# Kernel optimization log

Measured on AMD Instinct MI355X. Metric: run time of the kernel, lower is better.

Reference implementation:

```python
import jax, jax.numpy as jnp
import numpy as np

ENC, STR_H, CELL_H, ATTN = 512, 256, 512, 512
B, L = 64, 1024


def setup_inputs() -> dict:
    key = jax.random.key(0)
    ks = jax.random.split(key, 12)
    s = lambda fan_in: 1.0 / np.sqrt(fan_in)
    return {
        "encoded_features_map": jax.random.normal(ks[0], (B, L, ENC), jnp.float32),
        "structural_hidden_state": jax.random.normal(ks[1], (1, B, STR_H), jnp.float32),
        "cell_content_hidden_state": jax.random.normal(ks[2], (1, B, CELL_H), jnp.float32),
        "W_enc": jax.random.uniform(ks[3], (ENC, ATTN), jnp.float32, -s(ENC), s(ENC)),
        "b_enc": jax.random.uniform(ks[4], (ATTN,), jnp.float32, -s(ENC), s(ENC)),
        "W_str": jax.random.uniform(ks[5], (STR_H, ATTN), jnp.float32, -s(STR_H), s(STR_H)),
        "b_str": jax.random.uniform(ks[6], (ATTN,), jnp.float32, -s(STR_H), s(STR_H)),
        "W_cell": jax.random.uniform(ks[7], (CELL_H, ATTN), jnp.float32, -s(CELL_H), s(CELL_H)),
        "b_cell": jax.random.uniform(ks[8], (ATTN,), jnp.float32, -s(CELL_H), s(CELL_H)),
        "W_comb": jax.random.uniform(ks[9], (ATTN, 1), jnp.float32, -s(ATTN), s(ATTN)),
        "b_comb": jax.random.uniform(ks[10], (1,), jnp.float32, -s(ATTN), s(ATTN)),
    }


def reference(encoded_features_map, structural_hidden_state, cell_content_hidden_state,
              W_enc, b_enc, W_str, b_str, W_cell, b_cell, W_comb, b_comb):
    # [B, L, A] projection of encoder features
    a_enc = jnp.einsum("ble,ea->bla", encoded_features_map, W_enc) + b_enc
    # [B, A] projections of the two hidden states (squeeze layer dim)
    a_str = structural_hidden_state[0] @ W_str + b_str
    a_cell = cell_content_hidden_state[0] @ W_cell + b_cell
    # broadcast add + ReLU + scalar score: [B, L]
    h = jax.nn.relu(a_enc + a_str[:, None, :] + a_cell[:, None, :])
    scores = jnp.einsum("bla,ao->bl", h, W_comb) + b_comb[0]
    weights = jax.nn.softmax(scores, axis=1)  # over sequence dim
    # weighted sum over L -> [B, ENC]
    context = jnp.einsum("bl,ble->be", weights, encoded_features_map)
    return context
```

## Files before the change

kernel.cpp:

```cpp
#include <hip/hip_runtime.h>
#include <stdint.h>

#define ENC_D 512
#define ATTN_D 512
#define STR_D 256
#define CELL_D 512
#define BATCH 64
#define SEQ 1024
#define NROWS (BATCH * SEQ)

typedef __bf16 bf16x8 __attribute__((ext_vector_type(8)));
typedef float f32x4 __attribute__((ext_vector_type(4)));

__device__ __forceinline__ unsigned short f2bf(float f) {
    unsigned int u = __float_as_uint(f);
    u += 0x7fffu + ((u >> 16) & 1u);
    return (unsigned short)(u >> 16);
}

__device__ __forceinline__ void lds_cp16(void* l, const void* g) {
    __builtin_amdgcn_global_load_lds(
        (const __attribute__((address_space(1))) unsigned int*)g,
        (__attribute__((address_space(3))) unsigned int*)l, 16, 0, 0);
}

#define BAR_VM4() asm volatile("s_waitcnt vmcnt(4)\n\ts_barrier" ::: "memory")

__global__ __launch_bounds__(256) void k_prep(const float* __restrict__ W,
                                              unsigned short* __restrict__ WF,
                                              const float* __restrict__ str,
                                              const float* __restrict__ cell,
                                              const float* __restrict__ Wstr,
                                              const float* __restrict__ Wcell,
                                              float* __restrict__ bpart) {
    __shared__ char smraw[64 * 68 * 2];
    const int bx = blockIdx.x, t = threadIdx.x;

    if (bx < 64) {
        unsigned short* T = (unsigned short*)smraw;
        const int ei = bx >> 3, ni = bx & 7;
        const int e0 = ei * 64, n0 = ni * 64;
#pragma unroll
        for (int i = 0; i < 4; ++i) {
            const int idx = t + i * 256;
            const int r = idx >> 4, c4 = idx & 15;
            const float4 v = *(const float4*)(W + (size_t)(e0 + r) * ATTN_D + n0 + c4 * 4);
            T[(c4 * 4 + 0) * 68 + r] = f2bf(v.x);
            T[(c4 * 4 + 1) * 68 + r] = f2bf(v.y);
            T[(c4 * 4 + 2) * 68 + r] = f2bf(v.z);
            T[(c4 * 4 + 3) * 68 + r] = f2bf(v.w);
        }
        __syncthreads();
#pragma unroll
        for (int i = 0; i < 2; ++i) {
            const int q = t + i * 256;
            const int n = q >> 3, ge = q & 7;
            union { unsigned short s[8]; uint4 u; } o;
#pragma unroll
            for (int j = 0; j < 8; ++j) o.s[j] = T[n * 68 + ge * 8 + j];
            const int ng = n0 + n;
            const int g = ei * 8 + ge;
            const int nt = ng >> 4, c = ng & 15;
            const int ks = g >> 2, quad = g & 3;
            const int gi = ks * 2048 + nt * 64 + quad * 16 + c;
            *(uint4*)(WF + (size_t)gi * 8) = o.u;
        }
    } else {
        float* sj = (float*)smraw;
        float* red = (float*)smraw + 64;
        const int q = bx - 64;
        const int b = q / 12, jq = q - b * 12;
        const float* hvec;
        const float* Wbase;
        if (jq < 4) { hvec = str + b * STR_D + jq * 64;         Wbase = Wstr + (size_t)(jq * 64) * ATTN_D; }
        else        { hvec = cell + b * CELL_D + (jq - 4) * 64; Wbase = Wcell + (size_t)((jq - 4) * 64) * ATTN_D; }
        if (t < 64) sj[t] = hvec[t];
        __syncthreads();
        const int h = t >> 7, a4 = t & 127;
        f32x4 acc = {0.f, 0.f, 0.f, 0.f};
#pragma unroll 8
        for (int i = h * 32; i < h * 32 + 32; ++i) {
            const float s = sj[i];
            const float4 wv = *(const float4*)(Wbase + (size_t)i * ATTN_D + a4 * 4);
            acc[0] += s * wv.x; acc[1] += s * wv.y; acc[2] += s * wv.z; acc[3] += s * wv.w;
        }
        if (h == 1) *(f32x4*)(red + a4 * 4) = acc;
        __syncthreads();
        if (h == 0) {
            const f32x4 o = *(const f32x4*)(red + a4 * 4);
            acc[0] += o[0]; acc[1] += o[1]; acc[2] += o[2]; acc[3] += o[3];
            *(f32x4*)(bpart + (size_t)(jq * BATCH + b) * ATTN_D + a4 * 4) = acc;
        }
    }
}

__global__ __launch_bounds__(512, 2) void k_scores(const float* __restrict__ E,
                                                   const unsigned short* __restrict__ WF,
                                                   const float* __restrict__ bpart,
                                                   const float* __restrict__ b_enc,
                                                   const float* __restrict__ b_str,
                                                   const float* __restrict__ b_cell,
                                                   const float* __restrict__ Wcomb,
                                                   float* __restrict__ ctxp,
                                                   float* __restrict__ stats) {
    __shared__ unsigned short buf[3][16384];
    __shared__ float sbias[512];
    __shared__ float sWc[512];
    __shared__ float sxp[4][128];
    __shared__ float sx[128];
    __shared__ float ex[128];
    __shared__ float red[3][512];
    __shared__ float rtmp[4];

    const int tid = threadIdx.x;
    const int r0 = blockIdx.x * 128;
    const int b = blockIdx.x >> 3;
    const int w = tid >> 6, lane = tid & 63;
    const int wm = w >> 2, wn = w & 3;
    const int quad = lane >> 4, c = lane & 15;

#pragma unroll
    for (int p = 0; p < 2; ++p)
#pragma unroll
        for (int i = 0; i < 4; ++i)
            lds_cp16((char*)&buf[p][0] + i * 8192 + tid * 16,
                     (const char*)WF + (size_t)p * 32768 + i * 8192 + tid * 16);

    if (tid < 128) {
        const int a = tid * 4;
        const float4 be = *(const float4*)(b_enc + a);
        const float4 bs = *(const float4*)(b_str + a);
        const float4 bc = *(const float4*)(b_cell + a);
        f32x4 s;
        s[0] = be.x + bs.x + bc.x; s[1] = be.y + bs.y + bc.y;
        s[2] = be.z + bs.z + bc.z; s[3] = be.w + bs.w + bc.w;
#pragma unroll
        for (int jq = 0; jq < 12; ++jq) {
            const float4 p = *(const float4*)(bpart + (size_t)(jq * BATCH + b) * ATTN_D + a);
            s[0] += p.x; s[1] += p.y; s[2] += p.z; s[3] += p.w;
        }
        *(f32x4*)(sbias + a) = s;
        const float4 wcv = *(const float4*)(Wcomb + a);
        f32x4 wc4; wc4[0] = wcv.x; wc4[1] = wcv.y; wc4[2] = wcv.z; wc4[3] = wcv.w;
        *(f32x4*)(sWc + a) = wc4;
    }

    f32x4 acc[4][8];
#pragma unroll
    for (int mt = 0; mt < 4; ++mt)
#pragma unroll
        for (int nt = 0; nt < 8; ++nt) {
            const f32x4 z = {0.f, 0.f, 0.f, 0.f};
            acc[mt][nt] = z;
        }

    __syncthreads();

    const float* Ebase = E + (size_t)(r0 + wm * 64 + c) * ENC_D + quad * 8;

    int cbuf = 0, sbuf = 2;
    for (int ch = 0; ch < 16; ++ch) {
        float4 v0[4], v1[4];
#pragma unroll
        for (int mt = 0; mt < 4; ++mt) {
            const float* Ep = Ebase + (size_t)(mt * 16) * ENC_D + ch * 32;
            v0[mt] = *(const float4*)(Ep);
            v1[mt] = *(const float4*)(Ep + 4);
        }

        if (ch < 14) {
            const char* gsrc = (const char*)WF + (size_t)(ch + 2) * 32768;
            char* ldst = (char*)&buf[sbuf][0];
#pragma unroll
            for (int i = 0; i < 4; ++i)
                lds_cp16(ldst + i * 8192 + tid * 16, gsrc + i * 8192 + tid * 16);
        }

        bf16x8 av[4];
#pragma unroll
        for (int mt = 0; mt < 4; ++mt) {
            union { unsigned short s[8]; bf16x8 v; } u;
            u.s[0] = f2bf(v0[mt].x); u.s[1] = f2bf(v0[mt].y);
            u.s[2] = f2bf(v0[mt].z); u.s[3] = f2bf(v0[mt].w);
            u.s[4] = f2bf(v1[mt].x); u.s[5] = f2bf(v1[mt].y);
            u.s[6] = f2bf(v1[mt].z); u.s[7] = f2bf(v1[mt].w);
            av[mt] = u.v;
        }

        const unsigned short* wb = &buf[cbuf][0];
        bf16x8 bfr[8];
#pragma unroll
        for (int nt = 0; nt < 8; ++nt)
            bfr[nt] = *(const bf16x8*)(wb + ((wn * 8 + nt) * 64 + lane) * 8);
#pragma unroll
        for (int nt = 0; nt < 8; ++nt)
#pragma unroll
            for (int mt = 0; mt < 4; ++mt)
                acc[mt][nt] = __builtin_amdgcn_mfma_f32_16x16x32_bf16(av[mt], bfr[nt], acc[mt][nt], 0, 0, 0);

        cbuf = (cbuf == 2) ? 0 : cbuf + 1;
        sbuf = (sbuf == 2) ? 0 : sbuf + 1;
        if (ch < 15) BAR_VM4();
    }

    float sp[4][4];
#pragma unroll
    for (int mt = 0; mt < 4; ++mt)
#pragma unroll
        for (int reg = 0; reg < 4; ++reg) sp[mt][reg] = 0.f;
#pragma unroll
    for (int nt = 0; nt < 8; ++nt) {
        const int col = wn * 128 + nt * 16 + c;
        const float bi = sbias[col], wc = sWc[col];
#pragma unroll
        for (int mt = 0; mt < 4; ++mt)
#pragma unroll
            for (int reg = 0; reg < 4; ++reg) {
                const float v = acc[mt][nt][reg] + bi;
                sp[mt][reg] += (v > 0.f ? v : 0.f) * wc;
            }
    }
#pragma unroll
    for (int mt = 0; mt < 4; ++mt)
#pragma unroll
        for (int reg = 0; reg < 4; ++reg) {
            float v = sp[mt][reg];
            v += __shfl_xor(v, 1);
            v += __shfl_xor(v, 2);
            v += __shfl_xor(v, 4);
            v += __shfl_xor(v, 8);
            sp[mt][reg] = v;
        }
    if (c == 0) {
#pragma unroll
        for (int mt = 0; mt < 4; ++mt)
#pragma unroll
            for (int reg = 0; reg < 4; ++reg)
                sxp[wn][wm * 64 + mt * 16 + quad * 4 + reg] = sp[mt][reg];
    }
    __syncthreads();

    if (tid < 128)
        sx[tid] = sxp[0][tid] + sxp[1][tid] + sxp[2][tid] + sxp[3][tid];

    if (tid < 128) {
        float mm = sx[tid];
#pragma unroll
        for (int o = 32; o > 0; o >>= 1) mm = fmaxf(mm, __shfl_xor(mm, o));
        if (lane == 0) rtmp[w] = mm;
    }
    __syncthreads();
    const float m_p = fmaxf(rtmp[0], rtmp[1]);
    if (tid < 128) {
        const float e = __expf(sx[tid] - m_p);
        ex[tid] = e;
        float ss = e;
#pragma unroll
        for (int o = 32; o > 0; o >>= 1) ss += __shfl_xor(ss, o);
        if (lane == 0) rtmp[2 + w] = ss;
    }
    __syncthreads();
    if (tid == 0) {
        stats[blockIdx.x * 2 + 0] = m_p;
        stats[blockIdx.x * 2 + 1] = rtmp[2] + rtmp[3];
    }

    {
        const int g = tid >> 7, col4 = tid & 127;
        const float* Ep = E + (size_t)(r0 + g * 32) * ENC_D + col4 * 4;
        f32x4 a4 = {0.f, 0.f, 0.f, 0.f};
#pragma unroll 8
        for (int l = 0; l < 32; ++l) {
            const float4 e4 = *(const float4*)(Ep + (size_t)l * ENC_D);
            const float wgt = ex[g * 32 + l];
            a4[0] += wgt * e4.x; a4[1] += wgt * e4.y;
            a4[2] += wgt * e4.z; a4[3] += wgt * e4.w;
        }
        if (g > 0) *(f32x4*)(&red[g - 1][col4 * 4]) = a4;
        __syncthreads();
        if (g == 0) {
            const f32x4 r1 = *(const f32x4*)(&red[0][col4 * 4]);
            const f32x4 r2 = *(const f32x4*)(&red[1][col4 * 4]);
            const f32x4 r3 = *(const f32x4*)(&red[2][col4 * 4]);
            a4[0] += r1[0] + r2[0] + r3[0];
            a4[1] += r1[1] + r2[1] + r3[1];
            a4[2] += r1[2] + r2[2] + r3[2];
            a4[3] += r1[3] + r2[3] + r3[3];
            *(f32x4*)(ctxp + (size_t)blockIdx.x * 512 + col4 * 4) = a4;
        }
    }
}

__global__ __launch_bounds__(128) void k_final(const float* __restrict__ ctxp,
                                               const float* __restrict__ stats,
                                               float* __restrict__ out) {
    const int b = blockIdx.x, t = threadIdx.x;
    float mp[8], zp[8];
    float m = -1e30f;
#pragma unroll
    for (int p = 0; p < 8; ++p) {
        mp[p] = stats[(b * 8 + p) * 2];
        zp[p] = stats[(b * 8 + p) * 2 + 1];
        m = fmaxf(m, mp[p]);
    }
    float D = 0.f;
    float a[8];
#pragma unroll
    for (int p = 0; p < 8; ++p) { a[p] = __expf(mp[p] - m); D += zp[p] * a[p]; }
    const float invD = 1.f / D;

    f32x4 o = {0.f, 0.f, 0.f, 0.f};
#pragma unroll
    for (int p = 0; p < 8; ++p) {
        const float4 cp = *(const float4*)(ctxp + (size_t)(b * 8 + p) * 512 + t * 4);
        o[0] += cp.x * a[p]; o[1] += cp.y * a[p];
        o[2] += cp.z * a[p]; o[3] += cp.w * a[p];
    }
    o[0] *= invD; o[1] *= invD; o[2] *= invD; o[3] *= invD;
    *(f32x4*)(out + (size_t)b * ENC_D + t * 4) = o;
}

extern "C" void kernel_launch(void* const* d_in, const int* in_sizes, int n_in,
                              void* d_out, int out_size, void* d_ws, size_t ws_size,
                              hipStream_t stream) {
    const float* E      = (const float*)d_in[0];
    const float* str    = (const float*)d_in[1];
    const float* cell   = (const float*)d_in[2];
    const float* Wenc   = (const float*)d_in[3];
    const float* b_enc  = (const float*)d_in[4];
    const float* Wstr   = (const float*)d_in[5];
    const float* b_str  = (const float*)d_in[6];
    const float* Wcell  = (const float*)d_in[7];
    const float* b_cell = (const float*)d_in[8];
    const float* Wcomb  = (const float*)d_in[9];
    float* out = (float*)d_out;

    char* ws = (char*)d_ws;
    unsigned short* WF = (unsigned short*)ws;
    float* bpart = (float*)(ws + (512 << 10));
    float* ctxp  = (float*)(ws + (512 << 10) + (1536 << 10));
    float* stats = (float*)(ws + (512 << 10) + (2560 << 10));

    k_prep<<<832, 256, 0, stream>>>(Wenc, WF, str, cell, Wstr, Wcell, bpart);
    k_scores<<<NROWS / 128, 512, 0, stream>>>(E, WF, bpart, b_enc, b_str, b_cell, Wcomb, ctxp, stats);
    k_final<<<BATCH, 128, 0, stream>>>(ctxp, stats, out);
}
```

Before: 286.3 us.

## Double-buffer encoder activations in registers and use native bf16 conversion

Restructures the k_scores main loop so each chunk's fp32 encoder rows are loaded one chunk ahead into alternating register sets, and the loop is unrolled by two via a macro. The intent is to hide global load latency behind the MFMA work of the current chunk. The manual round-to-nearest-even bf16 packing is replaced with native `__bf16` casts to cut ALU work. The explicit `s_waitcnt vmcnt(4)` before the barrier is dropped and only a bare `s_barrier` remains, leaving LDS-DMA completion ordering to compiler-inserted waits. This risks a race on the weight staging buffers and raises register pressure from the extra prefetch registers.

After: 284.3 us. Within noise of the previous version (-0.7%).

```diff
diff --git a/kernel.cpp b/kernel.cpp
--- a/kernel.cpp
+++ b/kernel.cpp
@@ -18,13 +18,20 @@
     return (unsigned short)(u >> 16);
 }
 
+__device__ __forceinline__ bf16x8 cvt8(const float4 a, const float4 b) {
+    bf16x8 r;
+    r[0] = (__bf16)a.x; r[1] = (__bf16)a.y; r[2] = (__bf16)a.z; r[3] = (__bf16)a.w;
+    r[4] = (__bf16)b.x; r[5] = (__bf16)b.y; r[6] = (__bf16)b.z; r[7] = (__bf16)b.w;
+    return r;
+}
+
 __device__ __forceinline__ void lds_cp16(void* l, const void* g) {
     __builtin_amdgcn_global_load_lds(
         (const __attribute__((address_space(1))) unsigned int*)g,
         (__attribute__((address_space(3))) unsigned int*)l, 16, 0, 0);
 }
 
-#define BAR_VM4() asm volatile("s_waitcnt vmcnt(4)\n\ts_barrier" ::: "memory")
+#define BAR() asm volatile("s_barrier" ::: "memory")
 
 __global__ __launch_bounds__(256) void k_prep(const float* __restrict__ W,
                                               unsigned short* __restrict__ WF,
@@ -94,6 +101,40 @@
     }
 }
 
+#define CHUNK(ch, CUR0, CUR1, NXT0, NXT1, DO_STAGE, DO_PREF, DO_BAR)               \
+    do {                                                                           \
+        if (DO_STAGE) {                                                            \
+            const char* gsrc = (const char*)WF + (size_t)((ch) + 2) * 32768;       \
+            char* ldst = (char*)&buf[sbuf][0];                                     \
+            _Pragma("unroll")                                                      \
+            for (int i = 0; i < 4; ++i)                                            \
+                lds_cp16(ldst + i * 8192 + tid * 16, gsrc + i * 8192 + tid * 16);  \
+        }                                                                          \
+        if (DO_PREF) {                                                             \
+            _Pragma("unroll")                                                      \
+            for (int mt = 0; mt < 4; ++mt) {                                       \
+                const float* Ep = Ebase + (size_t)(mt * 16) * ENC_D + ((ch) + 1) * 32; \
+                NXT0[mt] = *(const float4*)(Ep);                                   \
+                NXT1[mt] = *(const float4*)(Ep + 4);                               \
+            }                                                                      \
+        }                                                                          \
+        bf16x8 av[4];                                                              \
+        _Pragma("unroll")                                                          \
+        for (int mt = 0; mt < 4; ++mt) av[mt] = cvt8(CUR0[mt], CUR1[mt]);          \
+        const unsigned short* wb = &buf[cbuf][0];                                  \
+        _Pragma("unroll")                                                          \
+        for (int nt = 0; nt < 8; ++nt) {                                           \
+            const bf16x8 bfr = *(const bf16x8*)(wb + ((wn * 8 + nt) * 64 + lane) * 8); \
+            _Pragma("unroll")                                                      \
+            for (int mt = 0; mt < 4; ++mt)                                         \
+                acc[mt][nt] = __builtin_amdgcn_mfma_f32_16x16x32_bf16(av[mt], bfr, \
+                                                        acc[mt][nt], 0, 0, 0);     \
+        }                                                                          \
+        cbuf = (cbuf == 2) ? 0 : cbuf + 1;                                         \
+        sbuf = (sbuf == 2) ? 0 : sbuf + 1;                                         \
+        if (DO_BAR) BAR();                                                         \
+    } while (0)
+
 __global__ __launch_bounds__(512, 2) void k_scores(const float* __restrict__ E,
                                                    const unsigned short* __restrict__ WF,
                                                    const float* __restrict__ bpart,
@@ -154,54 +195,25 @@
             acc[mt][nt] = z;
         }
 
+    const float* Ebase = E + (size_t)(r0 + wm * 64 + c) * ENC_D + quad * 8;
+
+    float4 pA0[4], pA1[4], pB0[4], pB1[4];
+#pragma unroll
+    for (int mt = 0; mt < 4; ++mt) {
+        const float* Ep = Ebase + (size_t)(mt * 16) * ENC_D;
+        pA0[mt] = *(const float4*)(Ep);
+        pA1[mt] = *(const float4*)(Ep + 4);
+    }
+
     __syncthreads();
 
-    const float* Ebase = E + (size_t)(r0 + wm * 64 + c) * ENC_D + quad * 8;
-
     int cbuf = 0, sbuf = 2;
-    for (int ch = 0; ch < 16; ++ch) {
-        float4 v0[4], v1[4];
-#pragma unroll
-        for (int mt = 0; mt < 4; ++mt) {
-            const float* Ep = Ebase + (size_t)(mt * 16) * ENC_D + ch * 32;
-            v0[mt] = *(const float4*)(Ep);
-            v1[mt] = *(const float4*)(Ep + 4);
-        }
-
-        if (ch < 14) {
-            const char* gsrc = (const char*)WF + (size_t)(ch + 2) * 32768;
-            char* ldst = (char*)&buf[sbuf][0];
-#pragma unroll
-            for (int i = 0; i < 4; ++i)
-                lds_cp16(ldst + i * 8192 + tid * 16, gsrc + i * 8192 + tid * 16);
-        }
-
-        bf16x8 av[4];
-#pragma unroll
-        for (int mt = 0; mt < 4; ++mt) {
-            union { unsigned short s[8]; bf16x8 v; } u;
-            u.s[0] = f2bf(v0[mt].x); u.s[1] = f2bf(v0[mt].y);
-            u.s[2] = f2bf(v0[mt].z); u.s[3] = f2bf(v0[mt].w);
-            u.s[4] = f2bf(v1[mt].x); u.s[5] = f2bf(v1[mt].y);
-            u.s[6] = f2bf(v1[mt].z); u.s[7] = f2bf(v1[mt].w);
-            av[mt] = u.v;
-        }
-
-        const unsigned short* wb = &buf[cbuf][0];
-        bf16x8 bfr[8];
-#pragma unroll
-        for (int nt = 0; nt < 8; ++nt)
-            bfr[nt] = *(const bf16x8*)(wb + ((wn * 8 + nt) * 64 + lane) * 8);
-#pragma unroll
-        for (int nt = 0; nt < 8; ++nt)
-#pragma unroll
-            for (int mt = 0; mt < 4; ++mt)
-                acc[mt][nt] = __builtin_amdgcn_mfma_f32_16x16x32_bf16(av[mt], bfr[nt], acc[mt][nt], 0, 0, 0);
-
-        cbuf = (cbuf == 2) ? 0 : cbuf + 1;
-        sbuf = (sbuf == 2) ? 0 : sbuf + 1;
-        if (ch < 15) BAR_VM4();
-    }
+    for (int cc = 0; cc < 14; cc += 2) {
+        CHUNK(cc,     pA0, pA1, pB0, pB1, true, true, true);
+        CHUNK(cc + 1, pB0, pB1, pA0, pA1, true, true, true);
+    }
+    CHUNK(14, pA0, pA1, pB0, pB1, false, true, true);
+    CHUNK(15, pB0, pB1, pA0, pA1, false, false, false);
 
     float sp[4][4];
 #pragma unroll
```
